# Optimization experiments

Hardware: AMD Instinct MI355X
Metric: run time of the kernel (lower is better)

## Reference

```python
import jax, jax.numpy as jnp
import numpy as np


def _rope(x, token_positions, theta):
    # x: [B, H, S, D], token_positions: [S]
    d = x.shape[-1]
    freqs = 1.0 / theta ** (jnp.arange(0, d, 2, dtype=jnp.float32) / d)  # [D/2]
    angles = token_positions.astype(jnp.float32)[:, None] * freqs[None, :]  # [S, D/2]
    cos, sin = jnp.cos(angles), jnp.sin(angles)
    x_even = x[..., 0::2]
    x_odd = x[..., 1::2]
    new_even = x_even * cos - x_odd * sin
    new_odd = x_even * sin + x_odd * cos
    return jnp.stack([new_even, new_odd], axis=-1).reshape(x.shape)


def setup_inputs() -> dict:
    key = jax.random.key(0)
    ks = jax.random.split(key, 5)
    B, S, D = 2, 2048, 1024
    scale = 1.0 / np.sqrt(D)
    return {
        "x": jax.random.normal(ks[0], (B, S, D), dtype=jnp.float32),
        "Wq": jax.random.normal(ks[1], (D, D), dtype=jnp.float32) * scale,
        "Wk": jax.random.normal(ks[2], (D, D), dtype=jnp.float32) * scale,
        "Wv": jax.random.normal(ks[3], (D, D), dtype=jnp.float32) * scale,
        "Wo": jax.random.normal(ks[4], (D, D), dtype=jnp.float32) * scale,
        "token_positions": jnp.arange(S, dtype=jnp.int32),
        "rope_theta": 10000,
    }


def reference(x, Wq, Wk, Wv, Wo, token_positions, rope_theta):
    B, S, Dm = x.shape
    H = 16
    d_k = Dm // H
    # nn.Linear(bias=False): y = x @ W.T
    def proj(W):
        y = jnp.einsum('bsd,ed->bse', x, W)
        return y.reshape(B, S, H, d_k).transpose(0, 2, 1, 3)  # [B,H,S,Dk]
    q = _rope(proj(Wq), token_positions, float(rope_theta))
    k = _rope(proj(Wk), token_positions, float(rope_theta))
    v = proj(Wv)
    scores = jnp.einsum('bhqd,bhkd->bhqk', q, k) / jnp.sqrt(jnp.float32(d_k))
    causal = jnp.tril(jnp.ones((S, S), dtype=bool))
    scores = jnp.where(causal, scores, -jnp.inf)
    p = jax.nn.softmax(scores, axis=-1)
    vals = jnp.einsum('bhqk,bhkd->bhqd', p, v)
    out = vals.transpose(0, 2, 1, 3).reshape(B, S, Dm)
    return jnp.einsum('bsd,ed->bse', out, Wo)
```

## Files before the change

kernel.cpp:

```cpp
#include <hip/hip_runtime.h>
#include <hip/hip_bf16.h>
#include <stdint.h>

typedef __attribute__((ext_vector_type(8))) __bf16 bf16x8;
typedef __attribute__((ext_vector_type(4))) float f32x4;
typedef __hip_bfloat16 bf16;

#define GLDS(g, l) __builtin_amdgcn_global_load_lds( \
    (const __attribute__((address_space(1))) void*)(g), \
    (__attribute__((address_space(3))) void*)(l), 16, 0, 0)

#define OFF_XB     ((size_t)0)
#define OFF_WQKVB  ((size_t)8388608)
#define OFF_WOB    ((size_t)14680064)
#define OFF_QB     ((size_t)16777216)
#define OFF_KB     ((size_t)25165824)
#define OFF_VTB    ((size_t)33554432)
#define OFF_CS     ((size_t)41943040)
#define OFF_SN     ((size_t)42205184)

__global__ void prep_kernel(const float* __restrict__ x, const float* __restrict__ wq,
                            const float* __restrict__ wk, const float* __restrict__ wv,
                            const float* __restrict__ wo,
                            bf16* __restrict__ xb, bf16* __restrict__ wqkvb,
                            bf16* __restrict__ wob)
{
    const int region = blockIdx.y;
    const float* src;
    bf16* dst;
    int count;
    switch (region) {
        case 0:  src = x;  dst = xb;              count = 4096 * 1024; break;
        case 1:  src = wq; dst = wqkvb;           count = 1024 * 1024; break;
        case 2:  src = wk; dst = wqkvb + 1048576; count = 1024 * 1024; break;
        case 3:  src = wv; dst = wqkvb + 2097152; count = 1024 * 1024; break;
        default: src = wo; dst = wob;             count = 1024 * 1024; break;
    }
    const int i = (blockIdx.x * 256 + threadIdx.x) * 4;
    if (i >= count) return;
    const float4 v = *(const float4*)(src + i);
    union { bf16 h[4]; short4 s4; } u;
    u.h[0] = __float2bfloat16(v.x);
    u.h[1] = __float2bfloat16(v.y);
    u.h[2] = __float2bfloat16(v.z);
    u.h[3] = __float2bfloat16(v.w);
    *(short4*)(dst + i) = u.s4;
}

__global__ void rope_table_kernel(const int* __restrict__ pos, const void* __restrict__ theta_p,
                                  float* __restrict__ cst, float* __restrict__ snt)
{
    const int t = blockIdx.x * 256 + threadIdx.x;
    const int s = t >> 5, i = t & 31;
    const int ti = ((const int*)theta_p)[0];
    const float theta = (ti > 0 && ti < 100000000) ? (float)ti : ((const float*)theta_p)[0];
    const float fr = expf(-(float)i * (1.0f / 32.0f) * logf(theta));
    const float ang = (float)pos[s] * fr;
    cst[t] = cosf(ang);
    snt[t] = sinf(ang);
}

template<int MODE>
__global__ __launch_bounds__(256) void gemm_bt(
    const bf16* __restrict__ A, const bf16* __restrict__ B,
    const int K, const int N,
    float* __restrict__ outf,
    bf16* __restrict__ qb, bf16* __restrict__ kb, bf16* __restrict__ vtb,
    const float* __restrict__ cst, const float* __restrict__ snt)
{
    __shared__ __align__(16) bf16 Asl[128 * 32];
    __shared__ __align__(16) bf16 Bsl[128 * 32];
    const int tid = threadIdx.x;
    const int wave = tid >> 6, lane = tid & 63;
    const int lr = lane & 15, lk = lane >> 4;
    const int m0 = blockIdx.x * 128;
    const int n0 = blockIdx.y * 128;
    const int wm = (wave >> 1) * 64;
    const int wn = (wave & 1) * 64;
    const int srow = tid >> 2, sseg = tid & 3;

    f32x4 acc[4][4] = {};

    const bf16* aRow = A + (size_t)(m0 + srow) * K + sseg * 8;
    const bf16* bRow = B + (size_t)(n0 + srow) * K + sseg * 8;
    char* lA = (char*)Asl + tid * 16;
    char* lB = (char*)Bsl + tid * 16;
    const size_t rowK64 = (size_t)64 * K;

    for (int k0 = 0; k0 < K; k0 += 32) {
        GLDS(aRow + k0, lA);
        GLDS(aRow + k0 + rowK64, lA + 4096);
        GLDS(bRow + k0, lB);
        GLDS(bRow + k0 + rowK64, lB + 4096);
        __syncthreads();
        bf16x8 af[4], bfr[4];
#pragma unroll
        for (int i = 0; i < 4; ++i)
            af[i] = *(const bf16x8*)(Asl + (wm + i * 16 + lr) * 32 + lk * 8);
#pragma unroll
        for (int j = 0; j < 4; ++j)
            bfr[j] = *(const bf16x8*)(Bsl + (wn + j * 16 + lr) * 32 + lk * 8);
#pragma unroll
        for (int i = 0; i < 4; ++i)
#pragma unroll
            for (int j = 0; j < 4; ++j)
                acc[i][j] = __builtin_amdgcn_mfma_f32_16x16x32_bf16(af[i], bfr[j], acc[i][j], 0, 0, 0);
        __syncthreads();
    }

    if constexpr (MODE == 1) {
#pragma unroll
        for (int i = 0; i < 4; ++i)
#pragma unroll
            for (int j = 0; j < 4; ++j)
#pragma unroll
                for (int r = 0; r < 4; ++r) {
                    const int row = m0 + wm + i * 16 + lk * 4 + r;
                    const int col = n0 + wn + j * 16 + lr;
                    outf[(size_t)row * N + col] = acc[i][j][r];
                }
    } else {
        const int matn = n0 >> 10;
#pragma unroll
        for (int i = 0; i < 4; ++i)
#pragma unroll
            for (int j = 0; j < 4; ++j)
#pragma unroll
                for (int r = 0; r < 4; ++r) {
                    const int row = m0 + wm + i * 16 + lk * 4 + r;
                    const int col = n0 + wn + j * 16 + lr;
                    float v = acc[i][j][r];
                    float p = __shfl_xor(v, 1);
                    const int e = col & 1023;
                    const int h = e >> 6;
                    const int dd = e & 63;
                    const int b = row >> 11;
                    const int s = row & 2047;
                    const size_t bhi = (size_t)(b * 16 + h);
                    if (matn == 2) {
                        vtb[(bhi * 64 + dd) * 2048 + s] = __float2bfloat16(v);
                    } else {
                        const float cs = cst[s * 32 + (dd >> 1)];
                        const float sn = snt[s * 32 + (dd >> 1)];
                        const float rv = (dd & 1) ? (p * sn + v * cs) : (v * cs - p * sn);
                        if (matn == 0)
                            qb[(bhi * 2048 + s) * 64 + dd] = __float2bfloat16(rv * 0.125f);
                        else
                            kb[(bhi * 2048 + s) * 64 + dd] = __float2bfloat16(rv);
                    }
                }
    }
}

__global__ __launch_bounds__(256) void attn_kernel(
    const bf16* __restrict__ qb, const bf16* __restrict__ kb,
    const bf16* __restrict__ vtb, bf16* __restrict__ attnb)
{
    __shared__ __align__(16) bf16 Kl[2][64 * 64];
    __shared__ __align__(16) bf16 Vl[2][64 * 64];
    __shared__ __align__(16) bf16 Pl[4][2][16][72];
    const int tid = threadIdx.x;
    const int wave = tid >> 6, lane = tid & 63;
    const int lr = lane & 15, lk = lane >> 4;
    const int tA = blockIdx.x;
    const int tB = 31 - tA;
    const int bh = blockIdx.y;
    const int qA = tA * 64 + wave * 16;
    const int qB = tB * 64 + wave * 16;

    const bf16* Qp = qb + (size_t)bh * 2048 * 64;
    const bf16* Kp = kb + (size_t)bh * 2048 * 64;
    const bf16* Vp = vtb + (size_t)bh * 64 * 2048;

    const int srow = tid >> 3;
    const int sseg = tid & 7;
    const int sw16 = (sseg ^ (srow & 7)) * 16;
    const char* kg = (const char*)Kp + (size_t)srow * 128 + sw16;
    const char* vg = (const char*)Vp + (size_t)srow * 4096 + sw16;

#define STAGE(kt_, c_) do {                                              \
        const char* kgt = kg + (size_t)(kt_) * 8192;                     \
        GLDS(kgt,              &Kl[c_][0] + tid * 8);                    \
        GLDS(kgt + 32 * 128,   &Kl[c_][0] + 2048 + tid * 8);             \
        const char* vgt = vg + (size_t)(kt_) * 128;                      \
        GLDS(vgt,              &Vl[c_][0] + tid * 8);                    \
        GLDS(vgt + 32 * 4096,  &Vl[c_][0] + 2048 + tid * 8);             \
    } while (0)

    bf16x8 qfA[2], qfB[2];
#pragma unroll
    for (int ks = 0; ks < 2; ++ks) {
        qfA[ks] = *(const bf16x8*)(Qp + (qA + lr) * 64 + ks * 32 + lk * 8);
        qfB[ks] = *(const bf16x8*)(Qp + (qB + lr) * 64 + ks * 32 + lk * 8);
    }

    float mA = -1e30f, mB = -1e30f, sA = 0.f, sB = 0.f;
    f32x4 oA[4] = {}, oB[4] = {};

    STAGE(0, 0);

    const int xoff = (lr & 7) * 8;

    for (int kt = 0; kt <= tB; ++kt) {
        const int c = kt & 1;
        const int kv0 = kt * 64;
        const bool doA = (kt <= tA);
        if (kt < tB) {
            STAGE(kt + 1, c ^ 1);
            asm volatile("s_waitcnt vmcnt(4)" ::: "memory");
        } else {
            asm volatile("s_waitcnt vmcnt(0)" ::: "memory");
        }
        __builtin_amdgcn_s_barrier();
        __builtin_amdgcn_sched_barrier(0);
        const bf16* Kc = &Kl[c][0];
        const bf16* Vc = &Vl[c][0];

        f32x4 scB[4] = {}, scA[4] = {};
#pragma unroll
        for (int ks = 0; ks < 2; ++ks) {
            bf16x8 kf[4];
#pragma unroll
            for (int j = 0; j < 4; ++j)
                kf[j] = *(const bf16x8*)(Kc + (j * 16 + lr) * 64 + ((ks * 32 + lk * 8) ^ xoff));
            __builtin_amdgcn_s_setprio(1);
#pragma unroll
            for (int j = 0; j < 4; ++j)
                scB[j] = __builtin_amdgcn_mfma_f32_16x16x32_bf16(kf[j], qfB[ks], scB[j], 0, 0, 0);
            if (doA) {
#pragma unroll
                for (int j = 0; j < 4; ++j)
                    scA[j] = __builtin_amdgcn_mfma_f32_16x16x32_bf16(kf[j], qfA[ks], scA[j], 0, 0, 0);
            }
            __builtin_amdgcn_s_setprio(0);
        }

        auto smx = [&](f32x4* sc, float& m, float& ssum, f32x4* o, int qX, bool diag, int st) {
            if (diag) {
#pragma unroll
                for (int j = 0; j < 4; ++j)
#pragma unroll
                    for (int r = 0; r < 4; ++r)
                        if (kv0 + j * 16 + lk * 4 + r > qX + lr) sc[j][r] = -1e30f;
            }
            float mt = sc[0][0];
#pragma unroll
            for (int j = 0; j < 4; ++j)
#pragma unroll
                for (int r = 0; r < 4; ++r) mt = fmaxf(mt, sc[j][r]);
            mt = fmaxf(mt, __shfl_xor(mt, 16));
            mt = fmaxf(mt, __shfl_xor(mt, 32));
            const float mn = fmaxf(m, mt);
            const float al = __expf(m - mn);
            m = mn;
            float ls = 0.f;
#pragma unroll
            for (int j = 0; j < 4; ++j) {
                float pv[4];
#pragma unroll
                for (int r = 0; r < 4; ++r) {
                    pv[r] = __expf(sc[j][r] - mn);
                    ls += pv[r];
                }
                union { bf16 h[4]; ushort4 s4; } u;
#pragma unroll
                for (int r = 0; r < 4; ++r) u.h[r] = __float2bfloat16(pv[r]);
                *(ushort4*)(&Pl[wave][st][lr][j * 16 + lk * 4]) = u.s4;
            }
            ssum = ssum * al + ls;
#pragma unroll
            for (int j = 0; j < 4; ++j)
#pragma unroll
                for (int r = 0; r < 4; ++r) o[j][r] *= al;
        };
        smx(scB, mB, sB, oB, qB, kt == tB, 1);
        if (doA) smx(scA, mA, sA, oA, qA, kt == tA, 0);

#pragma unroll
        for (int ks = 0; ks < 2; ++ks) {
            const bf16x8 pfB = *(const bf16x8*)(&Pl[wave][1][lr][ks * 32 + lk * 8]);
            bf16x8 pfA = pfB;
            if (doA) pfA = *(const bf16x8*)(&Pl[wave][0][lr][ks * 32 + lk * 8]);
            __builtin_amdgcn_s_setprio(1);
#pragma unroll
            for (int j = 0; j < 4; ++j) {
                bf16x8 vf = *(const bf16x8*)(Vc + (j * 16 + lr) * 64 + ((ks * 32 + lk * 8) ^ xoff));
                oB[j] = __builtin_amdgcn_mfma_f32_16x16x32_bf16(vf, pfB, oB[j], 0, 0, 0);
                if (doA)
                    oA[j] = __builtin_amdgcn_mfma_f32_16x16x32_bf16(vf, pfA, oA[j], 0, 0, 0);
            }
            __builtin_amdgcn_s_setprio(0);
        }
        __builtin_amdgcn_sched_barrier(0);
        __builtin_amdgcn_s_barrier();
    }

    const int b = bh >> 4, h = bh & 15;
    auto epi = [&](float ssum, f32x4* o, int qX) {
        float s = ssum;
        s += __shfl_xor(s, 16);
        s += __shfl_xor(s, 32);
        const float inv = 1.0f / s;
        const int qq = qX + lr;
        bf16* dst = attnb + (size_t)(b * 2048 + qq) * 1024 + h * 64 + lk * 4;
#pragma unroll
        for (int j = 0; j < 4; ++j) {
            union { bf16 h4[4]; ushort4 s4; } u;
#pragma unroll
            for (int r = 0; r < 4; ++r) u.h4[r] = __float2bfloat16(o[j][r] * inv);
            *(ushort4*)(dst + j * 16) = u.s4;
        }
    };
    epi(sA, oA, qA);
    epi(sB, oB, qB);
#undef STAGE
}

extern "C" void kernel_launch(void* const* d_in, const int* in_sizes, int n_in,
                              void* d_out, int out_size, void* d_ws, size_t ws_size,
                              hipStream_t stream)
{
    const float* x   = (const float*)d_in[0];
    const float* wq  = (const float*)d_in[1];
    const float* wk  = (const float*)d_in[2];
    const float* wv  = (const float*)d_in[3];
    const float* wo  = (const float*)d_in[4];
    const int*   pos = (const int*)d_in[5];
    const void* theta = d_in[6];

    char* ws = (char*)d_ws;
    bf16* xb    = (bf16*)(ws + OFF_XB);
    bf16* attnb = (bf16*)(ws + OFF_XB);
    bf16* wqkvb = (bf16*)(ws + OFF_WQKVB);
    bf16* wob   = (bf16*)(ws + OFF_WOB);
    bf16* qb    = (bf16*)(ws + OFF_QB);
    bf16* kb    = (bf16*)(ws + OFF_KB);
    bf16* vtb   = (bf16*)(ws + OFF_VTB);
    float* cst  = (float*)(ws + OFF_CS);
    float* snt  = (float*)(ws + OFF_SN);

    prep_kernel<<<dim3(4096, 5), 256, 0, stream>>>(x, wq, wk, wv, wo, xb, wqkvb, wob);
    rope_table_kernel<<<256, 256, 0, stream>>>(pos, theta, cst, snt);
    gemm_bt<0><<<dim3(32, 24), 256, 0, stream>>>(xb, wqkvb, 1024, 3072, nullptr,
                                                 qb, kb, vtb, cst, snt);
    attn_kernel<<<dim3(16, 32), 256, 0, stream>>>(qb, kb, vtb, attnb);
    gemm_bt<1><<<dim3(32, 8), 256, 0, stream>>>(attnb, wob, 1024, 1024, (float*)d_out,
                                                nullptr, nullptr, nullptr, nullptr, nullptr);
}
```

Before: 153.6 us.

## Swizzle GEMM LDS with K=64 tiles, remap workgroups, lazy softmax rescale

```diff
diff --git a/kernel.cpp b/kernel.cpp
--- a/kernel.cpp
+++ b/kernel.cpp
@@ -9,6 +9,8 @@
 #define GLDS(g, l) __builtin_amdgcn_global_load_lds( \
     (const __attribute__((address_space(1))) void*)(g), \
     (__attribute__((address_space(3))) void*)(l), 16, 0, 0)
+
+#define SCALE_Q 0.18033688f
 
 #define OFF_XB     ((size_t)0)
 #define OFF_WQKVB  ((size_t)8388608)
@@ -60,7 +62,7 @@
     snt[t] = sinf(ang);
 }
 
-template<int MODE>
+template<int MODE, int BM>
 __global__ __launch_bounds__(256) void gemm_bt(
     const bf16* __restrict__ A, const bf16* __restrict__ B,
     const int K, const int N,
@@ -68,49 +70,66 @@
     bf16* __restrict__ qb, bf16* __restrict__ kb, bf16* __restrict__ vtb,
     const float* __restrict__ cst, const float* __restrict__ snt)
 {
-    __shared__ __align__(16) bf16 Asl[128 * 32];
-    __shared__ __align__(16) bf16 Bsl[128 * 32];
+    constexpr int NF = BM / 32;
+    __shared__ __align__(16) bf16 Asl[BM * 64];
+    __shared__ __align__(16) bf16 Bsl[128 * 64];
     const int tid = threadIdx.x;
     const int wave = tid >> 6, lane = tid & 63;
     const int lr = lane & 15, lk = lane >> 4;
-    const int m0 = blockIdx.x * 128;
-    const int n0 = blockIdx.y * 128;
-    const int wm = (wave >> 1) * 64;
+
+    const int nwg = gridDim.x * gridDim.y;
+    const int flat = blockIdx.y * gridDim.x + blockIdx.x;
+    const int wg = (flat & 7) * (nwg >> 3) + (flat >> 3);
+    const int m0 = (wg % gridDim.x) * BM;
+    const int n0 = (wg / gridDim.x) * 128;
+
+    const int wm = (wave >> 1) * (BM / 2);
     const int wn = (wave & 1) * 64;
-    const int srow = tid >> 2, sseg = tid & 3;
-
-    f32x4 acc[4][4] = {};
-
-    const bf16* aRow = A + (size_t)(m0 + srow) * K + sseg * 8;
-    const bf16* bRow = B + (size_t)(n0 + srow) * K + sseg * 8;
+    const int srow = tid >> 3, sseg = tid & 7;
+    const int swel = (sseg ^ (srow & 7)) * 8;
+
+    f32x4 acc[NF][4] = {};
+
+    const bf16* aRow = A + (size_t)(m0 + srow) * K + swel;
+    const bf16* bRow = B + (size_t)(n0 + srow) * K + swel;
     char* lA = (char*)Asl + tid * 16;
     char* lB = (char*)Bsl + tid * 16;
-    const size_t rowK64 = (size_t)64 * K;
-
-    for (int k0 = 0; k0 < K; k0 += 32) {
-        GLDS(aRow + k0, lA);
-        GLDS(aRow + k0 + rowK64, lA + 4096);
-        GLDS(bRow + k0, lB);
-        GLDS(bRow + k0 + rowK64, lB + 4096);
+    const size_t rowK32 = (size_t)32 * K;
+
+    for (int k0 = 0; k0 < K; k0 += 64) {
+#pragma unroll
+        for (int g = 0; g < NF; ++g)
+            GLDS(aRow + k0 + g * rowK32, lA + g * 4096);
+#pragma unroll
+        for (int g = 0; g < 4; ++g)
+            GLDS(bRow + k0 + g * rowK32, lB + g * 4096);
         __syncthreads();
-        bf16x8 af[4], bfr[4];
-#pragma unroll
-        for (int i = 0; i < 4; ++i)
-            af[i] = *(const bf16x8*)(Asl + (wm + i * 16 + lr) * 32 + lk * 8);
-#pragma unroll
-        for (int j = 0; j < 4; ++j)
-            bfr[j] = *(const bf16x8*)(Bsl + (wn + j * 16 + lr) * 32 + lk * 8);
-#pragma unroll
-        for (int i = 0; i < 4; ++i)
-#pragma unroll
-            for (int j = 0; j < 4; ++j)
-                acc[i][j] = __builtin_amdgcn_mfma_f32_16x16x32_bf16(af[i], bfr[j], acc[i][j], 0, 0, 0);
+#pragma unroll
+        for (int kk = 0; kk < 2; ++kk) {
+            const int s = kk * 4 + lk;
+            bf16x8 af[NF], bfr[4];
+#pragma unroll
+            for (int i = 0; i < NF; ++i) {
+                const int R = wm + i * 16 + lr;
+                af[i] = *(const bf16x8*)((const char*)Asl + R * 128 + (((s) ^ (R & 7)) << 4));
+            }
+#pragma unroll
+            for (int j = 0; j < 4; ++j) {
+                const int R = wn + j * 16 + lr;
+                bfr[j] = *(const bf16x8*)((const char*)Bsl + R * 128 + (((s) ^ (R & 7)) << 4));
+            }
+#pragma unroll
+            for (int i = 0; i < NF; ++i)
+#pragma unroll
+                for (int j = 0; j < 4; ++j)
+                    acc[i][j] = __builtin_amdgcn_mfma_f32_16x16x32_bf16(af[i], bfr[j], acc[i][j], 0, 0, 0);
+        }
         __syncthreads();
     }
 
     if constexpr (MODE == 1) {
 #pragma unroll
-        for (int i = 0; i < 4; ++i)
+        for (int i = 0; i < NF; ++i)
 #pragma unroll
             for (int j = 0; j < 4; ++j)
 #pragma unroll
@@ -122,7 +141,7 @@
     } else {
         const int matn = n0 >> 10;
 #pragma unroll
-        for (int i = 0; i < 4; ++i)
+        for (int i = 0; i < NF; ++i)
 #pragma unroll
             for (int j = 0; j < 4; ++j)
 #pragma unroll
@@ -144,7 +163,7 @@
                         const float sn = snt[s * 32 + (dd >> 1)];
                         const float rv = (dd & 1) ? (p * sn + v * cs) : (v * cs - p * sn);
                         if (matn == 0)
-                            qb[(bhi * 2048 + s) * 64 + dd] = __float2bfloat16(rv * 0.125f);
+                            qb[(bhi * 2048 + s) * 64 + dd] = __float2bfloat16(rv * SCALE_Q);
                         else
                             kb[(bhi * 2048 + s) * 64 + dd] = __float2bfloat16(rv);
                     }
@@ -250,16 +269,23 @@
                 for (int r = 0; r < 4; ++r) mt = fmaxf(mt, sc[j][r]);
             mt = fmaxf(mt, __shfl_xor(mt, 16));
             mt = fmaxf(mt, __shfl_xor(mt, 32));
-            const float mn = fmaxf(m, mt);
-            const float al = __expf(m - mn);
-            m = mn;
+            if (!__all(mt <= m + 8.0f)) {
+                const float mn = fmaxf(m, mt);
+                const float al = exp2f(m - mn);
+                m = mn;
+                ssum *= al;
+#pragma unroll
+                for (int j = 0; j < 4; ++j)
+#pragma unroll
+                    for (int r = 0; r < 4; ++r) o[j][r] *= al;
+            }
             float ls = 0.f;
 #pragma unroll
             for (int j = 0; j < 4; ++j) {
                 float pv[4];
 #pragma unroll
                 for (int r = 0; r < 4; ++r) {
-                    pv[r] = __expf(sc[j][r] - mn);
+                    pv[r] = exp2f(sc[j][r] - m);
                     ls += pv[r];
                 }
                 union { bf16 h[4]; ushort4 s4; } u;
@@ -267,11 +293,7 @@
                 for (int r = 0; r < 4; ++r) u.h[r] = __float2bfloat16(pv[r]);
                 *(ushort4*)(&Pl[wave][st][lr][j * 16 + lk * 4]) = u.s4;
             }
-            ssum = ssum * al + ls;
-#pragma unroll
-            for (int j = 0; j < 4; ++j)
-#pragma unroll
-                for (int r = 0; r < 4; ++r) o[j][r] *= al;
+            ssum += ls;
         };
         smx(scB, mB, sB, oB, qB, kt == tB, 1);
         if (doA) smx(scA, mA, sA, oA, qA, kt == tA, 0);
@@ -341,9 +363,9 @@
 
     prep_kernel<<<dim3(4096, 5), 256, 0, stream>>>(x, wq, wk, wv, wo, xb, wqkvb, wob);
     rope_table_kernel<<<256, 256, 0, stream>>>(pos, theta, cst, snt);
-    gemm_bt<0><<<dim3(32, 24), 256, 0, stream>>>(xb, wqkvb, 1024, 3072, nullptr,
-                                                 qb, kb, vtb, cst, snt);
+    gemm_bt<0, 128><<<dim3(32, 24), 256, 0, stream>>>(xb, wqkvb, 1024, 3072, nullptr,
+                                                      qb, kb, vtb, cst, snt);
     attn_kernel<<<dim3(16, 32), 256, 0, stream>>>(qb, kb, vtb, attnb);
-    gemm_bt<1><<<dim3(32, 8), 256, 0, stream>>>(attnb, wob, 1024, 1024, (float*)d_out,
-                                                nullptr, nullptr, nullptr, nullptr, nullptr);
-}
+    gemm_bt<1, 64><<<dim3(64, 8), 256, 0, stream>>>(attnb, wob, 1024, 1024, (float*)d_out,
+                                                    nullptr, nullptr, nullptr, nullptr, nullptr);
+}
```

Measured after the change: 154.0 us. No clear change (+0.2%).
